# Optimization experiments

Measured on AMD Instinct MI355X. Metric: run time of the kernel, lower is better.

The kernel has to match this reference:

```python
import jax, jax.numpy as jnp
import numpy as np
import math

B, T, C, H = 2, 2048, 1024, 16
HD = C // H

def setup_inputs() -> dict:
    key = jax.random.key(0)
    ks = jax.random.split(key, 5)
    s_in = 1.0 / math.sqrt(C)
    x = jax.random.normal(ks[0], (B, T, C), dtype=jnp.float32)
    W_attn = jax.random.normal(ks[1], (C, 3 * C), dtype=jnp.float32) * s_in
    b_attn = jnp.zeros((3 * C,), dtype=jnp.float32)
    W_proj = jax.random.normal(ks[2], (C, C), dtype=jnp.float32) * s_in
    b_proj = jnp.zeros((C,), dtype=jnp.float32)
    return {"x": x, "W_attn": W_attn, "b_attn": b_attn, "W_proj": W_proj, "b_proj": b_proj}

def reference(x, W_attn, b_attn, W_proj, b_proj):
    Bx, Tx, Cx = x.shape
    c = x @ W_attn + b_attn  # [B,T,3C]
    q, k, v = jnp.split(c, 3, axis=2)
    # [B,T,H,hd] -> [B,H,T,hd]
    q = q.reshape(Bx, Tx, H, HD).transpose(0, 2, 1, 3)
    k = k.reshape(Bx, Tx, H, HD).transpose(0, 2, 1, 3)
    v = v.reshape(Bx, Tx, H, HD).transpose(0, 2, 1, 3)
    # NOTE: module scales by 1/sqrt(C), not 1/sqrt(head_dim)
    attn = jnp.einsum('bhqd,bhkd->bhqk', q, k) * (1.0 / math.sqrt(Cx))
    causal = jnp.tril(jnp.ones((Tx, Tx), dtype=bool))
    attn = jnp.where(causal[None, None], attn, -jnp.inf)
    attn = jax.nn.softmax(attn, axis=-1)
    y = jnp.einsum('bhqk,bhkd->bhqd', attn, v)
    y = y.transpose(0, 2, 1, 3).reshape(Bx, Tx, Cx)
    return y @ W_proj + b_proj
```

## Files before the change

### kernel.cpp

```cpp
#include <hip/hip_runtime.h>
#include <math.h>

#define Bv 2
#define Tv 2048
#define Cv 1024
#define Hv 16
#define HDv 64
#define Mv (Bv * Tv)
#define SZv (Bv * Hv * Tv * HDv)

typedef short bf16x8 __attribute__((ext_vector_type(8)));
typedef float f32x4 __attribute__((ext_vector_type(4)));

static __device__ __forceinline__ unsigned short f2bf(float f) {
    unsigned u = __float_as_uint(f);
    u += 0x7fffu + ((u >> 16) & 1u);
    return (unsigned short)(u >> 16);
}

static __device__ __forceinline__ unsigned f2bf2(float a, float b) {
    unsigned r;
    asm("v_cvt_pk_bf16_f32 %0, %1, %2" : "=v"(r) : "v"(a), "v"(b));
    return r;
}

#define AS1 __attribute__((address_space(1)))
#define AS3 __attribute__((address_space(3)))
#define GLD16(gp, lp) __builtin_amdgcn_global_load_lds( \
    (AS1 const void*)(const void*)(gp), (AS3 void*)(void*)(lp), 16, 0, 0)

#define WAITVM(n) asm volatile("s_waitcnt vmcnt(" #n ")" ::: "memory")
#define WAITLGKM0 asm volatile("s_waitcnt lgkmcnt(0)" ::: "memory")
#define BARRIER   asm volatile("s_barrier" ::: "memory")

__global__ __launch_bounds__(256) void prep_kernel(
    const float* __restrict__ x, const float* __restrict__ Wa,
    const float* __restrict__ Wp,
    unsigned short* __restrict__ xB, unsigned short* __restrict__ WaT,
    unsigned short* __restrict__ WpT)
{
    __shared__ float tile[32][33];
    const int bid = blockIdx.x;
    const int tid = threadIdx.x;

    if (bid < 4096) {
        int i = bid * 256 + tid;
        float4 f = ((const float4*)x)[i];
        ushort4 u;
        u.x = f2bf(f.x); u.y = f2bf(f.y); u.z = f2bf(f.z); u.w = f2bf(f.w);
        ((ushort4*)xB)[i] = u;
        return;
    }
    const float* src; unsigned short* dst; int Ncols, bi;
    if (bid < 7168) { bi = bid - 4096; Ncols = 3072; src = Wa; dst = WaT; }
    else            { bi = bid - 7168; Ncols = 1024; src = Wp; dst = WpT; }
    const int nct = Ncols / 32;
    const int c0 = (bi % nct) * 32, r0 = (bi / nct) * 32;
    const int tx = tid & 31, ty = tid >> 5;
    #pragma unroll
    for (int i = 0; i < 4; ++i)
        tile[ty + i * 8][tx] = src[(size_t)(r0 + ty + i * 8) * Ncols + c0 + tx];
    __syncthreads();
    #pragma unroll
    for (int i = 0; i < 4; ++i)
        dst[(size_t)(c0 + ty + i * 8) * Cv + r0 + tx] = f2bf(tile[tx][ty + i * 8]);
}

__device__ __forceinline__ void mm_mainloop_1024(
    const unsigned short* __restrict__ A, const unsigned short* __restrict__ Bt,
    unsigned short* lds, int rowBase, int colBase, f32x4 acc[4][4])
{
    const int tid  = threadIdx.x;
    const int lane = tid & 63;
    const int w    = tid >> 6;
    const int quad = lane >> 4, l15 = lane & 15;
    const int wm = (w >> 1) * 64, wn = (w & 1) * 64;
    const int K = 1024;

    const int g0 = (w * 2 + 0) * 64 + lane;
    const int g1 = (w * 2 + 1) * 64 + lane;
    const int r0 = g0 >> 2, r1 = g1 >> 2;
    const int kc0 = (g0 & 3) ^ ((r0 >> 1) & 3);
    const int kc1 = (g1 & 3) ^ ((r1 >> 1) & 3);
    const size_t offA0 = (size_t)(rowBase + r0) * K + kc0 * 8;
    const size_t offA1 = (size_t)(rowBase + r1) * K + kc1 * 8;
    const size_t offB0 = (size_t)(colBase + r0) * K + kc0 * 8;
    const size_t offB1 = (size_t)(colBase + r1) * K + kc1 * 8;
    unsigned short* ldsA0 = lds + (w * 2 + 0) * 512;
    unsigned short* ldsA1 = lds + (w * 2 + 1) * 512;
    unsigned short* ldsB0 = lds + 4096 + (w * 2 + 0) * 512;
    unsigned short* ldsB1 = lds + 4096 + (w * 2 + 1) * 512;

    const int sw = quad ^ ((l15 >> 1) & 3);
    int aoff[4], boff[4];
    #pragma unroll
    for (int i = 0; i < 4; ++i) {
        aoff[i] = ((wm + i * 16 + l15) * 4 + sw) * 8;
        boff[i] = 4096 + ((wn + i * 16 + l15) * 4 + sw) * 8;
    }

    GLD16(A + offA0, ldsA0);
    GLD16(A + offA1, ldsA1);
    GLD16(Bt + offB0, ldsB0);
    GLD16(Bt + offB1, ldsB1);
    GLD16(A + offA0 + 32, ldsA0 + 8192);
    GLD16(A + offA1 + 32, ldsA1 + 8192);
    GLD16(Bt + offB0 + 32, ldsB0 + 8192);
    GLD16(Bt + offB1 + 32, ldsB1 + 8192);

    int cur = 0;
    for (int i = 0; i < 32; ++i) {
        if (i < 31) { WAITVM(4); } else { WAITVM(0); }
        BARRIER;
        if (i < 30) {
            int nb = cur + 16384; if (nb >= 24576) nb -= 24576;
            const int k2 = (i + 2) * 32;
            GLD16(A + offA0 + k2, ldsA0 + nb);
            GLD16(A + offA1 + k2, ldsA1 + nb);
            GLD16(Bt + offB0 + k2, ldsB0 + nb);
            GLD16(Bt + offB1 + k2, ldsB1 + nb);
        }

        bf16x8 a[4], b[4];
        #pragma unroll
        for (int j = 0; j < 4; ++j) a[j] = *(const bf16x8*)(lds + cur + aoff[j]);
        #pragma unroll
        for (int j = 0; j < 4; ++j) b[j] = *(const bf16x8*)(lds + cur + boff[j]);

        #pragma unroll
        for (int mi = 0; mi < 4; ++mi)
            #pragma unroll
            for (int ni = 0; ni < 4; ++ni)
                acc[mi][ni] = __builtin_amdgcn_mfma_f32_16x16x32_bf16(
                    a[mi], b[ni], acc[mi][ni], 0, 0, 0);

        cur += 8192; if (cur == 24576) cur = 0;
    }
}

__global__ __launch_bounds__(256) void qkv_mm_kernel(
    const unsigned short* __restrict__ xB, const unsigned short* __restrict__ WaT,
    const float* __restrict__ bias,
    unsigned short* __restrict__ qB, unsigned short* __restrict__ kB,
    unsigned short* __restrict__ vT)
{
    __shared__ __align__(16) unsigned short lds[24576];
    const int rowBase = blockIdx.y * 128;
    const int colBase = blockIdx.x * 128;

    f32x4 acc[4][4];
    #pragma unroll
    for (int i = 0; i < 4; ++i)
        #pragma unroll
        for (int j = 0; j < 4; ++j) acc[i][j] = (f32x4){0.f, 0.f, 0.f, 0.f};

    mm_mainloop_1024(xB, WaT, lds, rowBase, colBase, acc);
    __syncthreads();

    const int tid = threadIdx.x, lane = tid & 63, w = tid >> 6;
    const int quad = lane >> 4, l15 = lane & 15;
    const int wm = (w >> 1) * 64, wn = (w & 1) * 64;
    const int s = colBase / Cv;
    const int tloc = rowBase & (Tv - 1);
    const int bh0 = (rowBase / Tv) * Hv + (colBase % Cv) / HDv;

    if (s < 2) {
        const float qs = (s == 0) ? 0.04508422f : 1.0f;
        #pragma unroll
        for (int mi = 0; mi < 4; ++mi)
            #pragma unroll
            for (int ni = 0; ni < 4; ++ni) {
                float bv = bias[colBase + wn + ni * 16 + l15];
                #pragma unroll
                for (int r = 0; r < 4; ++r) {
                    int m = wm + mi * 16 + quad * 4 + r;
                    int n = wn + ni * 16 + l15;
                    lds[m * 136 + n] = f2bf((acc[mi][ni][r] + bv) * qs);
                }
            }
        __syncthreads();
        unsigned short* dst = (s == 0) ? qB : kB;
        #pragma unroll
        for (int it = 0; it < 8; ++it) {
            int cc = tid + it * 256;
            int m = cc >> 4, j = cc & 15;
            uint4 v = *(const uint4*)(lds + m * 136 + j * 8);
            int hh = j >> 3, d0 = (j & 7) * 8;
            *(uint4*)(dst + ((size_t)(bh0 + hh) * Tv + tloc + m) * HDv + d0) = v;
        }
    } else {
        #pragma unroll
        for (int mi = 0; mi < 4; ++mi)
            #pragma unroll
            for (int ni = 0; ni < 4; ++ni) {
                float bv = bias[colBase + wn + ni * 16 + l15];
                #pragma unroll
                for (int r = 0; r < 4; ++r) {
                    int m = wm + mi * 16 + quad * 4 + r;
                    int n = wn + ni * 16 + l15;
                    lds[n * 136 + m] = f2bf(acc[mi][ni][r] + bv);
                }
            }
        __syncthreads();
        #pragma unroll
        for (int it = 0; it < 8; ++it) {
            int cc = tid + it * 256;
            int n = cc >> 4, j = cc & 15;
            uint4 v = *(const uint4*)(lds + n * 136 + j * 8);
            int hh = n >> 6, d = n & 63;
            *(uint4*)(vT + ((size_t)(bh0 + hh) * HDv + d) * Tv + tloc + j * 8) = v;
        }
    }
}

__global__ __launch_bounds__(256) void proj_mm_kernel(
    const unsigned short* __restrict__ y0B, const unsigned short* __restrict__ WpT,
    const float* __restrict__ bias, float* __restrict__ out)
{
    __shared__ __align__(16) unsigned short lds[24576];
    const int rowBase = blockIdx.y * 128;
    const int colBase = blockIdx.x * 128;

    f32x4 acc[4][4];
    #pragma unroll
    for (int i = 0; i < 4; ++i)
        #pragma unroll
        for (int j = 0; j < 4; ++j) acc[i][j] = (f32x4){0.f, 0.f, 0.f, 0.f};

    mm_mainloop_1024(y0B, WpT, lds, rowBase, colBase, acc);

    const int tid = threadIdx.x, lane = tid & 63, w = tid >> 6;
    const int quad = lane >> 4, l15 = lane & 15;
    const int wm = (w >> 1) * 64, wn = (w & 1) * 64;

    #pragma unroll
    for (int mi = 0; mi < 4; ++mi)
        #pragma unroll
        for (int ni = 0; ni < 4; ++ni) {
            int n = colBase + wn + ni * 16 + l15;
            float bv = bias[n];
            #pragma unroll
            for (int r = 0; r < 4; ++r) {
                int m = rowBase + wm + mi * 16 + quad * 4 + r;
                out[(size_t)m * Cv + n] = acc[mi][ni][r] + bv;
            }
        }
}

__global__ __launch_bounds__(256) void attn_kernel(
    const unsigned short* __restrict__ qB, const unsigned short* __restrict__ kB,
    const unsigned short* __restrict__ vT, unsigned short* __restrict__ y0B)
{
    __shared__ __align__(16) unsigned short kv[2 * 8192];
    __shared__ __align__(16) unsigned short Pb[4][16 * 72];

    const int tid  = threadIdx.x;
    const int lane = tid & 63;
    const int w    = tid >> 6;
    const int quad = lane >> 4;
    const int l15  = lane & 15;

    const int qt = 31 - (blockIdx.x >> 5);
    const int bh = blockIdx.x & 31;
    const int qwbase = qt * 64 + w * 16;

    const unsigned short* qrow = qB + ((size_t)bh * Tv + qwbase + l15) * HDv;
    const bf16x8 Qa0 = *(const bf16x8*)(qrow + quad * 8);
    const bf16x8 Qa1 = *(const bf16x8*)(qrow + 32 + quad * 8);
    WAITVM(0);

    f32x4 O[4];
    float l[4] = {0.f, 0.f, 0.f, 0.f};
    #pragma unroll
    for (int n = 0; n < 4; ++n) O[n] = (f32x4){0.f, 0.f, 0.f, 0.f};

    const unsigned short* Kbase = kB + (size_t)bh * Tv * HDv;
    const unsigned short* Vbase = vT + (size_t)bh * HDv * Tv;
    unsigned short* Pw = &Pb[w][0];

    const unsigned short* gK[2]; unsigned short* dK[2];
    const unsigned short* gV[2]; unsigned short* dV[2];
    #pragma unroll
    for (int i = 0; i < 2; ++i) {
        int slot = tid + i * 256;
        int row = slot >> 3;
        int gk = (slot & 7) ^ ((row >> 2) & 7);
        gK[i] = Kbase + row * HDv + gk * 8;
        dK[i] = kv + (size_t)(i * 256 + w * 64) * 8;
        int d = slot >> 3;
        int gv = (slot & 7) ^ (d & 7);
        gV[i] = Vbase + (size_t)d * Tv + gv * 8;
        dV[i] = kv + 4096 + (size_t)(i * 256 + w * 64) * 8;
    }

    int koff[4][2], voff[4][2];
    #pragma unroll
    for (int ct = 0; ct < 4; ++ct) {
        int row = ct + 4 * l15;
        #pragma unroll
        for (int j = 0; j < 2; ++j)
            koff[ct][j] = (row * 8 + ((quad + 4 * j) ^ (l15 & 7))) * 8;
    }
    #pragma unroll
    for (int nt = 0; nt < 4; ++nt) {
        int d = nt * 16 + l15;
        #pragma unroll
        for (int j = 0; j < 2; ++j)
            voff[nt][j] = 4096 + (d * 8 + ((quad + 4 * j) ^ (l15 & 7))) * 8;
    }

    GLD16(gK[0], dK[0]);
    GLD16(gK[1], dK[1]);
    GLD16(gV[0], dV[0]);
    GLD16(gV[1], dV[1]);

    int cur = 0;
    for (int kt = 0; kt <= qt; ++kt) {
        WAITVM(0);
        BARRIER;
        if (kt < qt) {
            const int kb1 = (kt + 1) * 64;
            const int nxt = 8192 - cur;
            GLD16(gK[0] + (size_t)kb1 * HDv, dK[0] + nxt);
            GLD16(gK[1] + (size_t)kb1 * HDv, dK[1] + nxt);
            GLD16(gV[0] + kb1, dV[0] + nxt);
            GLD16(gV[1] + kb1, dV[1] + nxt);
        }

        bf16x8 Kb[4][2], Vb[4][2];
        #pragma unroll
        for (int ct = 0; ct < 4; ++ct) {
            Kb[ct][0] = *(const bf16x8*)(kv + cur + koff[ct][0]);
            Kb[ct][1] = *(const bf16x8*)(kv + cur + koff[ct][1]);
        }
        #pragma unroll
        for (int nt = 0; nt < 4; ++nt) {
            Vb[nt][0] = *(const bf16x8*)(kv + cur + voff[nt][0]);
            Vb[nt][1] = *(const bf16x8*)(kv + cur + voff[nt][1]);
        }

        f32x4 S[4];
        #pragma unroll
        for (int ct = 0; ct < 4; ++ct) {
            S[ct] = (f32x4){0.f, 0.f, 0.f, 0.f};
            S[ct] = __builtin_amdgcn_mfma_f32_16x16x32_bf16(Qa0, Kb[ct][0], S[ct], 0, 0, 0);
            S[ct] = __builtin_amdgcn_mfma_f32_16x16x32_bf16(Qa1, Kb[ct][1], S[ct], 0, 0, 0);
        }

        if (kt == qt) {
            #pragma unroll
            for (int ct = 0; ct < 4; ++ct)
                #pragma unroll
                for (int r = 0; r < 4; ++r)
                    if (ct + 4 * l15 > w * 16 + quad * 4 + r) S[ct][r] = -1e30f;
        }

        float p[4][4];
        #pragma unroll
        for (int ct = 0; ct < 4; ++ct)
            #pragma unroll
            for (int r = 0; r < 4; ++r)
                p[ct][r] = __builtin_amdgcn_exp2f(S[ct][r]);
        #pragma unroll
        for (int r = 0; r < 4; ++r)
            l[r] += (p[0][r] + p[1][r]) + (p[2][r] + p[3][r]);

        #pragma unroll
        for (int r = 0; r < 4; ++r) {
            uint2 u = make_uint2(f2bf2(p[0][r], p[1][r]), f2bf2(p[2][r], p[3][r]));
            *(uint2*)(Pw + (quad * 4 + r) * 72 + l15 * 4) = u;
        }
        WAITLGKM0;
        const bf16x8 Pa0 = *(const bf16x8*)(Pw + l15 * 72 + quad * 8);
        const bf16x8 Pa1 = *(const bf16x8*)(Pw + l15 * 72 + 32 + quad * 8);

        #pragma unroll
        for (int nt = 0; nt < 4; ++nt) {
            O[nt] = __builtin_amdgcn_mfma_f32_16x16x32_bf16(Pa0, Vb[nt][0], O[nt], 0, 0, 0);
            O[nt] = __builtin_amdgcn_mfma_f32_16x16x32_bf16(Pa1, Vb[nt][1], O[nt], 0, 0, 0);
        }

        cur = 8192 - cur;
    }

    #pragma unroll
    for (int r = 0; r < 4; ++r) {
        l[r] += __shfl_xor(l[r], 1);
        l[r] += __shfl_xor(l[r], 2);
        l[r] += __shfl_xor(l[r], 4);
        l[r] += __shfl_xor(l[r], 8);
    }

    const int b = bh >> 4, h = bh & 15;
    #pragma unroll
    for (int r = 0; r < 4; ++r) {
        float inv = 1.f / l[r];
        int q = qwbase + quad * 4 + r;
        unsigned short* dst = y0B + ((size_t)(b * Tv + q)) * Cv + h * HDv + l15;
        #pragma unroll
        for (int n = 0; n < 4; ++n) dst[n * 16] = f2bf(O[n][r] * inv);
    }
}

extern "C" void kernel_launch(void* const* d_in, const int* in_sizes, int n_in,
                              void* d_out, int out_size, void* d_ws, size_t ws_size,
                              hipStream_t stream) {
    const float* x      = (const float*)d_in[0];
    const float* W_attn = (const float*)d_in[1];
    const float* b_attn = (const float*)d_in[2];
    const float* W_proj = (const float*)d_in[3];
    const float* b_proj = (const float*)d_in[4];
    float* out = (float*)d_out;

    unsigned short* xB  = (unsigned short*)d_ws;
    unsigned short* WaT = xB  + (size_t)Mv * Cv;
    unsigned short* WpT = WaT + (size_t)3 * Cv * Cv;
    unsigned short* qB  = WpT + (size_t)Cv * Cv;
    unsigned short* kB  = qB + (size_t)SZv;
    unsigned short* vT  = kB + (size_t)SZv;
    unsigned short* y0B = vT + (size_t)SZv;

    dim3 blk(256);
    prep_kernel<<<dim3(8192), blk, 0, stream>>>(x, W_attn, W_proj, xB, WaT, WpT);
    qkv_mm_kernel<<<dim3(3 * Cv / 128, Mv / 128), blk, 0, stream>>>(xB, WaT, b_attn, qB, kB, vT);
    attn_kernel<<<dim3(Bv * Hv * (Tv / 64)), blk, 0, stream>>>(qB, kB, vT, y0B);
    proj_mm_kernel<<<dim3(Cv / 128, Mv / 128), blk, 0, stream>>>(y0B, WpT, b_proj, out);
}
```

Before: 169.2 us.

## Process 128 query rows per attention block, two 16-row subtiles per wave

Each attention block now covers 128 query rows instead of 64, and each wave handles two 16-row query subtiles. Every K/V tile loaded into shared memory therefore serves twice as many queries, halving total K/V global and LDS traffic. The cost is half as many blocks (512), more registers per wave, wasted masked work on the two diagonal tiles, and coarser causal load balance.

Result: slower. 179.0 us (+5.8%).

```diff
diff --git a/kernel.cpp b/kernel.cpp
--- a/kernel.cpp
+++ b/kernel.cpp
@@ -252,7 +252,7 @@
     const unsigned short* __restrict__ vT, unsigned short* __restrict__ y0B)
 {
     __shared__ __align__(16) unsigned short kv[2 * 8192];
-    __shared__ __align__(16) unsigned short Pb[4][16 * 72];
+    __shared__ __align__(16) unsigned short Pb[4][32 * 72];
 
     const int tid  = threadIdx.x;
     const int lane = tid & 63;
@@ -260,19 +260,25 @@
     const int quad = lane >> 4;
     const int l15  = lane & 15;
 
-    const int qt = 31 - (blockIdx.x >> 5);
+    const int qt = 15 - (blockIdx.x >> 5);
     const int bh = blockIdx.x & 31;
-    const int qwbase = qt * 64 + w * 16;
-
-    const unsigned short* qrow = qB + ((size_t)bh * Tv + qwbase + l15) * HDv;
-    const bf16x8 Qa0 = *(const bf16x8*)(qrow + quad * 8);
-    const bf16x8 Qa1 = *(const bf16x8*)(qrow + 32 + quad * 8);
+    const int qbase = qt * 128 + w * 32;
+
+    bf16x8 Qa[2][2];
+    #pragma unroll
+    for (int s = 0; s < 2; ++s) {
+        const unsigned short* qrow = qB + ((size_t)bh * Tv + qbase + s * 16 + l15) * HDv;
+        Qa[s][0] = *(const bf16x8*)(qrow + quad * 8);
+        Qa[s][1] = *(const bf16x8*)(qrow + 32 + quad * 8);
+    }
     WAITVM(0);
 
-    f32x4 O[4];
-    float l[4] = {0.f, 0.f, 0.f, 0.f};
-    #pragma unroll
-    for (int n = 0; n < 4; ++n) O[n] = (f32x4){0.f, 0.f, 0.f, 0.f};
+    f32x4 O[2][4];
+    float l[2][4];
+    #pragma unroll
+    for (int s = 0; s < 2; ++s)
+        #pragma unroll
+        for (int n = 0; n < 4; ++n) { O[s][n] = (f32x4){0.f, 0.f, 0.f, 0.f}; l[s][n] = 0.f; }
 
     const unsigned short* Kbase = kB + (size_t)bh * Tv * HDv;
     const unsigned short* Vbase = vT + (size_t)bh * HDv * Tv;
@@ -309,16 +315,18 @@
             voff[nt][j] = 4096 + (d * 8 + ((quad + 4 * j) ^ (l15 & 7))) * 8;
     }
 
+    const int numT = 2 * qt + 2;
+
     GLD16(gK[0], dK[0]);
     GLD16(gK[1], dK[1]);
     GLD16(gV[0], dV[0]);
     GLD16(gV[1], dV[1]);
 
     int cur = 0;
-    for (int kt = 0; kt <= qt; ++kt) {
+    for (int kt = 0; kt < numT; ++kt) {
         WAITVM(0);
         BARRIER;
-        if (kt < qt) {
+        if (kt + 1 < numT) {
             const int kb1 = (kt + 1) * 64;
             const int nxt = 8192 - cur;
             GLD16(gK[0] + (size_t)kb1 * HDv, dK[0] + nxt);
@@ -339,67 +347,85 @@
             Vb[nt][1] = *(const bf16x8*)(kv + cur + voff[nt][1]);
         }
 
-        f32x4 S[4];
-        #pragma unroll
-        for (int ct = 0; ct < 4; ++ct) {
-            S[ct] = (f32x4){0.f, 0.f, 0.f, 0.f};
-            S[ct] = __builtin_amdgcn_mfma_f32_16x16x32_bf16(Qa0, Kb[ct][0], S[ct], 0, 0, 0);
-            S[ct] = __builtin_amdgcn_mfma_f32_16x16x32_bf16(Qa1, Kb[ct][1], S[ct], 0, 0, 0);
-        }
-
-        if (kt == qt) {
+        f32x4 S[2][4];
+        #pragma unroll
+        for (int s = 0; s < 2; ++s)
+            #pragma unroll
+            for (int ct = 0; ct < 4; ++ct) {
+                S[s][ct] = (f32x4){0.f, 0.f, 0.f, 0.f};
+                S[s][ct] = __builtin_amdgcn_mfma_f32_16x16x32_bf16(Qa[s][0], Kb[ct][0], S[s][ct], 0, 0, 0);
+                S[s][ct] = __builtin_amdgcn_mfma_f32_16x16x32_bf16(Qa[s][1], Kb[ct][1], S[s][ct], 0, 0, 0);
+            }
+
+        if (kt >= numT - 2) {
+            const int kb = kt * 64;
+            #pragma unroll
+            for (int s = 0; s < 2; ++s)
+                #pragma unroll
+                for (int ct = 0; ct < 4; ++ct)
+                    #pragma unroll
+                    for (int r = 0; r < 4; ++r)
+                        if (kb + ct + 4 * l15 > qbase + s * 16 + quad * 4 + r)
+                            S[s][ct][r] = -1e30f;
+        }
+
+        float p[2][4][4];
+        #pragma unroll
+        for (int s = 0; s < 2; ++s) {
             #pragma unroll
             for (int ct = 0; ct < 4; ++ct)
                 #pragma unroll
                 for (int r = 0; r < 4; ++r)
-                    if (ct + 4 * l15 > w * 16 + quad * 4 + r) S[ct][r] = -1e30f;
-        }
-
-        float p[4][4];
-        #pragma unroll
-        for (int ct = 0; ct < 4; ++ct)
+                    p[s][ct][r] = __builtin_amdgcn_exp2f(S[s][ct][r]);
             #pragma unroll
             for (int r = 0; r < 4; ++r)
-                p[ct][r] = __builtin_amdgcn_exp2f(S[ct][r]);
-        #pragma unroll
-        for (int r = 0; r < 4; ++r)
-            l[r] += (p[0][r] + p[1][r]) + (p[2][r] + p[3][r]);
-
+                l[s][r] += (p[s][0][r] + p[s][1][r]) + (p[s][2][r] + p[s][3][r]);
+        }
+
+        #pragma unroll
+        for (int s = 0; s < 2; ++s)
+            #pragma unroll
+            for (int r = 0; r < 4; ++r) {
+                uint2 u = make_uint2(f2bf2(p[s][0][r], p[s][1][r]),
+                                     f2bf2(p[s][2][r], p[s][3][r]));
+                *(uint2*)(Pw + (s * 16 + quad * 4 + r) * 72 + l15 * 4) = u;
+            }
+        WAITLGKM0;
+        #pragma unroll
+        for (int s = 0; s < 2; ++s) {
+            const bf16x8 Pa0 = *(const bf16x8*)(Pw + (s * 16 + l15) * 72 + quad * 8);
+            const bf16x8 Pa1 = *(const bf16x8*)(Pw + (s * 16 + l15) * 72 + 32 + quad * 8);
+            #pragma unroll
+            for (int nt = 0; nt < 4; ++nt) {
+                O[s][nt] = __builtin_amdgcn_mfma_f32_16x16x32_bf16(Pa0, Vb[nt][0], O[s][nt], 0, 0, 0);
+                O[s][nt] = __builtin_amdgcn_mfma_f32_16x16x32_bf16(Pa1, Vb[nt][1], O[s][nt], 0, 0, 0);
+            }
+        }
+
+        cur = 8192 - cur;
+    }
+
+    #pragma unroll
+    for (int s = 0; s < 2; ++s)
         #pragma unroll
         for (int r = 0; r < 4; ++r) {
-            uint2 u = make_uint2(f2bf2(p[0][r], p[1][r]), f2bf2(p[2][r], p[3][r]));
-            *(uint2*)(Pw + (quad * 4 + r) * 72 + l15 * 4) = u;
-        }
-        WAITLGKM0;
-        const bf16x8 Pa0 = *(const bf16x8*)(Pw + l15 * 72 + quad * 8);
-        const bf16x8 Pa1 = *(const bf16x8*)(Pw + l15 * 72 + 32 + quad * 8);
-
-        #pragma unroll
-        for (int nt = 0; nt < 4; ++nt) {
-            O[nt] = __builtin_amdgcn_mfma_f32_16x16x32_bf16(Pa0, Vb[nt][0], O[nt], 0, 0, 0);
-            O[nt] = __builtin_amdgcn_mfma_f32_16x16x32_bf16(Pa1, Vb[nt][1], O[nt], 0, 0, 0);
-        }
-
-        cur = 8192 - cur;
-    }
-
-    #pragma unroll
-    for (int r = 0; r < 4; ++r) {
-        l[r] += __shfl_xor(l[r], 1);
-        l[r] += __shfl_xor(l[r], 2);
-        l[r] += __shfl_xor(l[r], 4);
-        l[r] += __shfl_xor(l[r], 8);
-    }
+            l[s][r] += __shfl_xor(l[s][r], 1);
+            l[s][r] += __shfl_xor(l[s][r], 2);
+            l[s][r] += __shfl_xor(l[s][r], 4);
+            l[s][r] += __shfl_xor(l[s][r], 8);
+        }
 
     const int b = bh >> 4, h = bh & 15;
     #pragma unroll
-    for (int r = 0; r < 4; ++r) {
-        float inv = 1.f / l[r];
-        int q = qwbase + quad * 4 + r;
-        unsigned short* dst = y0B + ((size_t)(b * Tv + q)) * Cv + h * HDv + l15;
-        #pragma unroll
-        for (int n = 0; n < 4; ++n) dst[n * 16] = f2bf(O[n][r] * inv);
-    }
+    for (int s = 0; s < 2; ++s)
+        #pragma unroll
+        for (int r = 0; r < 4; ++r) {
+            float inv = 1.f / l[s][r];
+            int q = qbase + s * 16 + quad * 4 + r;
+            unsigned short* dst = y0B + ((size_t)(b * Tv + q)) * Cv + h * HDv + l15;
+            #pragma unroll
+            for (int n = 0; n < 4; ++n) dst[n * 16] = f2bf(O[s][n][r] * inv);
+        }
 }
 
 extern "C" void kernel_launch(void* const* d_in, const int* in_sizes, int n_in,
@@ -423,6 +449,6 @@
     dim3 blk(256);
     prep_kernel<<<dim3(8192), blk, 0, stream>>>(x, W_attn, W_proj, xB, WaT, WpT);
     qkv_mm_kernel<<<dim3(3 * Cv / 128, Mv / 128), blk, 0, stream>>>(xB, WaT, b_attn, qB, kB, vT);
-    attn_kernel<<<dim3(Bv * Hv * (Tv / 64)), blk, 0, stream>>>(qB, kB, vT, y0B);
+    attn_kernel<<<dim3(Bv * Hv * (Tv / 128)), blk, 0, stream>>>(qB, kB, vT, y0B);
     proj_mm_kernel<<<dim3(Cv / 128, Mv / 128), blk, 0, stream>>>(y0B, WpT, b_proj, out);
 }
```

## Software-pipeline attention PV matmul one tile behind QK with double-buffered P

Applied to the files above, without the earlier changes.

Restructures the attention loop so the P·V MFMAs for the previous key tile run at the start of the next iteration, overlapping with the QK MFMAs and exp of the current tile. The P buffer in LDS is double-buffered and V fragments are held in registers across iterations, which removes the wait between writing P to LDS and reading it back. A final epilogue applies the last tile's P·V. It also adds a launch bound of three blocks per CU, which together with the extra V registers may force spills or reduce unrolling freedom.

New measurement: 163.6 us. 1.03x faster.

```diff
diff --git a/kernel.cpp b/kernel.cpp
--- a/kernel.cpp
+++ b/kernel.cpp
@@ -247,12 +247,12 @@
         }
 }
 
-__global__ __launch_bounds__(256) void attn_kernel(
+__global__ __launch_bounds__(256, 3) void attn_kernel(
     const unsigned short* __restrict__ qB, const unsigned short* __restrict__ kB,
     const unsigned short* __restrict__ vT, unsigned short* __restrict__ y0B)
 {
     __shared__ __align__(16) unsigned short kv[2 * 8192];
-    __shared__ __align__(16) unsigned short Pb[4][16 * 72];
+    __shared__ __align__(16) unsigned short Pb[2][4][16 * 72];
 
     const int tid  = threadIdx.x;
     const int lane = tid & 63;
@@ -276,7 +276,8 @@
 
     const unsigned short* Kbase = kB + (size_t)bh * Tv * HDv;
     const unsigned short* Vbase = vT + (size_t)bh * HDv * Tv;
-    unsigned short* Pw = &Pb[w][0];
+    unsigned short* Pw0 = &Pb[0][w][0];
+    unsigned short* Pw1 = &Pb[1][w][0];
 
     const unsigned short* gK[2]; unsigned short* dK[2];
     const unsigned short* gV[2]; unsigned short* dV[2];
@@ -314,6 +315,7 @@
     GLD16(gV[0], dV[0]);
     GLD16(gV[1], dV[1]);
 
+    bf16x8 Vprev[4][2];
     int cur = 0;
     for (int kt = 0; kt <= qt; ++kt) {
         WAITVM(0);
@@ -327,18 +329,25 @@
             GLD16(gV[1] + kb1, dV[1] + nxt);
         }
 
-        bf16x8 Kb[4][2], Vb[4][2];
+        unsigned short* PwW = (kt & 1) ? Pw1 : Pw0;
+        unsigned short* PwR = (kt & 1) ? Pw0 : Pw1;
+
+        if (kt > 0) {
+            const bf16x8 Pa0 = *(const bf16x8*)(PwR + l15 * 72 + quad * 8);
+            const bf16x8 Pa1 = *(const bf16x8*)(PwR + l15 * 72 + 32 + quad * 8);
+            #pragma unroll
+            for (int nt = 0; nt < 4; ++nt) {
+                O[nt] = __builtin_amdgcn_mfma_f32_16x16x32_bf16(Pa0, Vprev[nt][0], O[nt], 0, 0, 0);
+                O[nt] = __builtin_amdgcn_mfma_f32_16x16x32_bf16(Pa1, Vprev[nt][1], O[nt], 0, 0, 0);
+            }
+        }
+
+        bf16x8 Kb[4][2];
         #pragma unroll
         for (int ct = 0; ct < 4; ++ct) {
             Kb[ct][0] = *(const bf16x8*)(kv + cur + koff[ct][0]);
             Kb[ct][1] = *(const bf16x8*)(kv + cur + koff[ct][1]);
         }
-        #pragma unroll
-        for (int nt = 0; nt < 4; ++nt) {
-            Vb[nt][0] = *(const bf16x8*)(kv + cur + voff[nt][0]);
-            Vb[nt][1] = *(const bf16x8*)(kv + cur + voff[nt][1]);
-        }
-
         f32x4 S[4];
         #pragma unroll
         for (int ct = 0; ct < 4; ++ct) {
@@ -347,6 +356,12 @@
             S[ct] = __builtin_amdgcn_mfma_f32_16x16x32_bf16(Qa1, Kb[ct][1], S[ct], 0, 0, 0);
         }
 
+        #pragma unroll
+        for (int nt = 0; nt < 4; ++nt) {
+            Vprev[nt][0] = *(const bf16x8*)(kv + cur + voff[nt][0]);
+            Vprev[nt][1] = *(const bf16x8*)(kv + cur + voff[nt][1]);
+        }
+
         if (kt == qt) {
             #pragma unroll
             for (int ct = 0; ct < 4; ++ct)
@@ -368,19 +383,21 @@
         #pragma unroll
         for (int r = 0; r < 4; ++r) {
             uint2 u = make_uint2(f2bf2(p[0][r], p[1][r]), f2bf2(p[2][r], p[3][r]));
-            *(uint2*)(Pw + (quad * 4 + r) * 72 + l15 * 4) = u;
-        }
-        WAITLGKM0;
-        const bf16x8 Pa0 = *(const bf16x8*)(Pw + l15 * 72 + quad * 8);
-        const bf16x8 Pa1 = *(const bf16x8*)(Pw + l15 * 72 + 32 + quad * 8);
-
+            *(uint2*)(PwW + (quad * 4 + r) * 72 + l15 * 4) = u;
+        }
+
+        cur = 8192 - cur;
+    }
+
+    {
+        unsigned short* PwR = (qt & 1) ? Pw1 : Pw0;
+        const bf16x8 Pa0 = *(const bf16x8*)(PwR + l15 * 72 + quad * 8);
+        const bf16x8 Pa1 = *(const bf16x8*)(PwR + l15 * 72 + 32 + quad * 8);
         #pragma unroll
         for (int nt = 0; nt < 4; ++nt) {
-            O[nt] = __builtin_amdgcn_mfma_f32_16x16x32_bf16(Pa0, Vb[nt][0], O[nt], 0, 0, 0);
-            O[nt] = __builtin_amdgcn_mfma_f32_16x16x32_bf16(Pa1, Vb[nt][1], O[nt], 0, 0, 0);
-        }
-
-        cur = 8192 - cur;
+            O[nt] = __builtin_amdgcn_mfma_f32_16x16x32_bf16(Pa0, Vprev[nt][0], O[nt], 0, 0, 0);
+            O[nt] = __builtin_amdgcn_mfma_f32_16x16x32_bf16(Pa1, Vprev[nt][1], O[nt], 0, 0, 0);
+        }
     }
 
     #pragma unroll
```
